# Kernel optimization log

Measured on AMD Instinct MI355X. Metric: run time of the kernel, lower is better.

## Reference

```python
import jax, jax.numpy as jnp
import numpy as np

B, D = 1024, 768


def setup_inputs() -> dict:
    key = jax.random.key(0)
    k1, k2 = jax.random.split(key)
    image_features = jax.random.normal(k1, (B, D), dtype=jnp.float32)
    # plant a few exact duplicate rows so the label-propagation path is nontrivial
    image_features = image_features.at[17].set(image_features[3])
    image_features = image_features.at[512].set(image_features[3])
    image_features = image_features.at[900].set(image_features[128])
    text_features = jax.random.normal(k2, (B, D), dtype=jnp.float32)
    logit_scale = jnp.float32(14.285714)  # exp(log(1/0.07)), standard CLIP init
    return {"image_features": image_features, "text_features": text_features, "logit_scale": logit_scale}


def reference(image_features, text_features, logit_scale):
    # logits_per_image: [B, B]
    logits = logit_scale * (image_features @ text_features.T)
    # Duplicate detection: the original O(B^2) python loop assigns to row j the
    # index of the FIRST row i (i <= j) whose features exactly equal row j.
    # eq[i, j] = rows i and j are elementwise identical
    eq = jnp.all(image_features[:, None, :] == image_features[None, :, :], axis=-1)  # [B, B] bool
    labels = jnp.argmax(eq, axis=0)  # first matching index per row (diag guarantees a hit)
    # cross-entropy with integer labels, mean over batch
    logp = jax.nn.log_softmax(logits, axis=1)
    loss = -jnp.mean(jnp.take_along_axis(logp, labels[:, None], axis=1))
    return loss
```

## Files before the change

kernel.cpp:

```cpp
#include <hip/hip_runtime.h>
#include <stdint.h>

#define BATCH 1024
#define DIM 768

typedef unsigned long long u64;
typedef __attribute__((ext_vector_type(8))) short short8;
typedef __attribute__((ext_vector_type(4))) float f32x4;

#define WS_TAIL     0
#define WS_PMAX  4096
#define WS_PSUM 20480
#define WS_LVAL 36864
#define WS_TXTB 49152

__device__ __forceinline__ unsigned short to_bf16(float x) {
    unsigned int u = __float_as_uint(x);
    return (unsigned short)((u + 0x7FFFu + ((u >> 16) & 1u)) >> 16);
}

__global__ __launch_bounds__(256) void prep_kernel(
        const float* __restrict__ txt, int* __restrict__ tailcnt,
        unsigned short* __restrict__ txtB) {
    if (blockIdx.x == 0 && threadIdx.x == 0) { *tailcnt = 0; }
    const int wave = threadIdx.x >> 6;
    const int lane = threadIdx.x & 63;

    for (int i = wave; i < 6; i += 4) {
        const int G  = blockIdx.x * 6 + i;
        const int tt = G / 24;
        const int g  = G - tt * 24;
        const int col = tt * 16 + (lane & 15);
        const int k0  = g * 32 + (lane >> 4) * 8;
        const float4 va = *(const float4*)(txt + (size_t)col * DIM + k0);
        const float4 vb = *(const float4*)(txt + (size_t)col * DIM + k0 + 4);
        short8 hv = {(short)to_bf16(va.x), (short)to_bf16(va.y),
                     (short)to_bf16(va.z), (short)to_bf16(va.w),
                     (short)to_bf16(vb.x), (short)to_bf16(vb.y),
                     (short)to_bf16(vb.z), (short)to_bf16(vb.w)};
        *(short8*)(txtB + (size_t)(g * 64 + tt) * 512 + lane * 8) = hv;
    }
}

__global__ __launch_bounds__(1024) void gemm_fused(
        const float* __restrict__ img, const float* __restrict__ txt,
        const float* __restrict__ scale_p, const unsigned short* __restrict__ txtB,
        float* __restrict__ pmax, float* __restrict__ psum,
        float* __restrict__ lval, int* __restrict__ tailcnt,
        float* __restrict__ out) {
    __shared__ unsigned short Ahi[16 * DIM];
    __shared__ float logitsS[16 * 260];
    __shared__ int isLast;
    __shared__ float part[16];

    const int tid  = threadIdx.x;
    const int wave = tid >> 6;
    const int lane = tid & 63;
    const int quad = lane >> 4;
    const int l15  = lane & 15;
    const int r0    = (blockIdx.x >> 2) * 16;
    const int chunk = blockIdx.x & 3;

    {
        const float* ir = img + (size_t)(r0 + wave) * DIM;
#pragma unroll
        for (int j = 0; j < 12; ++j) {
            const int k = lane + j * 64;
            Ahi[((k >> 3) * 16 + wave) * 8 + (k & 7)] = to_bf16(ir[k]);
        }
    }
    __syncthreads();

    const int t = chunk * 16 + wave;
    const int foff = quad * 128 + l15 * 8;
    f32x4 acc = {0.f, 0.f, 0.f, 0.f};
#pragma unroll
    for (int kk = 0; kk < 24; ++kk) {
        const short8 a = *(const short8*)&Ahi[kk * 512 + foff];
        const short8 b = *(const short8*)(txtB + (size_t)(kk * 64 + t) * 512 + foff);
        acc = __builtin_amdgcn_mfma_f32_16x16x32_bf16(a, b, acc, 0, 0, 0);
    }

    const float scale = scale_p[0];
#pragma unroll
    for (int r = 0; r < 4; ++r)
        logitsS[(quad * 4 + r) * 260 + wave * 16 + l15] = scale * acc[r];
    __syncthreads();

    {
        const float4 f = *(const float4*)&logitsS[wave * 260 + lane * 4];
        float mx = fmaxf(fmaxf(f.x, f.y), fmaxf(f.z, f.w));
#pragma unroll
        for (int s = 32; s; s >>= 1) mx = fmaxf(mx, __shfl_xor(mx, s, 64));
        float sum = __expf(f.x - mx) + __expf(f.y - mx) +
                    __expf(f.z - mx) + __expf(f.w - mx);
#pragma unroll
        for (int s = 32; s; s >>= 1) sum += __shfl_xor(sum, s, 64);
        if (lane == 0) {
            atomicExch(&pmax[(r0 + wave) * 4 + chunk], mx);
            atomicExch(&psum[(r0 + wave) * 4 + chunk], sum);
        }
    }

    if (wave < 4) {
        const int j = r0 + chunk * 4 + wave;
        const float2 sj = *(const float2*)(img + (size_t)j * DIM);
        int lo = -1;
        int label = j;
        for (;;) {
            int cand = BATCH;
#pragma unroll
            for (int it = 0; it < 16; ++it) {
                const int i = lane + it * 64;
                const float2 si = *(const float2*)(img + (size_t)i * DIM);
                if (i < j && i > lo && si.x == sj.x && si.y == sj.y)
                    cand = min(cand, i);
            }
#pragma unroll
            for (int s = 32; s; s >>= 1) cand = min(cand, __shfl_xor(cand, s, 64));
            if (cand >= j) break;
            const float4* rpm = (const float4*)(img + (size_t)cand * DIM);
            const float4* rpj = (const float4*)(img + (size_t)j * DIM);
            bool eq = true;
#pragma unroll
            for (int cc = 0; cc < 3; ++cc) {
                float4 vm = rpm[cc * 64 + lane];
                float4 vj = rpj[cc * 64 + lane];
                eq = eq && (vm.x == vj.x) && (vm.y == vj.y) &&
                     (vm.z == vj.z) && (vm.w == vj.w);
            }
            if (__all(eq)) { label = cand; break; }
            lo = cand;
        }

        const float4* aj = (const float4*)(img + (size_t)j * DIM);
        const float4* bl = (const float4*)(txt + (size_t)label * DIM);
        float s = 0.0f;
#pragma unroll
        for (int cc = 0; cc < 3; ++cc) {
            const float4 va = aj[cc * 64 + lane];
            const float4 vb = bl[cc * 64 + lane];
            s += va.x * vb.x + va.y * vb.y + va.z * vb.z + va.w * vb.w;
        }
#pragma unroll
        for (int m = 32; m; m >>= 1) s += __shfl_xor(s, m, 64);
        if (lane == 0) atomicExch(&lval[j], scale * s);
    }

    __syncthreads();
    if (tid == 0)
        isLast = (atomicAdd(tailcnt, 1) == (int)gridDim.x - 1) ? 1 : 0;
    __syncthreads();
    if (!isLast) return;
    __threadfence();

    {
        const float4 m4 = *(const float4*)&pmax[tid * 4];
        const float4 s4 = *(const float4*)&psum[tid * 4];
        const float lv = lval[tid];
        const float gmax = fmaxf(fmaxf(m4.x, m4.y), fmaxf(m4.z, m4.w));
        const float ss = s4.x * __expf(m4.x - gmax) + s4.y * __expf(m4.y - gmax)
                       + s4.z * __expf(m4.z - gmax) + s4.w * __expf(m4.w - gmax);
        float loss = gmax + __logf(ss) - lv;
#pragma unroll
        for (int m = 32; m; m >>= 1) loss += __shfl_xor(loss, m, 64);
        if (lane == 0) part[wave] = loss;
        __syncthreads();
        if (tid == 0) {
            float tot = 0.0f;
#pragma unroll
            for (int w = 0; w < 16; ++w) tot += part[w];
            out[0] = tot * (1.0f / BATCH);
        }
    }
}

extern "C" void kernel_launch(void* const* d_in, const int* in_sizes, int n_in,
                              void* d_out, int out_size, void* d_ws, size_t ws_size,
                              hipStream_t stream) {
    const float* img   = (const float*)d_in[0];
    const float* txt   = (const float*)d_in[1];
    const float* scale = (const float*)d_in[2];
    float* out = (float*)d_out;
    char* ws = (char*)d_ws;

    int*   tailcnt = (int*)(ws + WS_TAIL);
    float* pmax    = (float*)(ws + WS_PMAX);
    float* psum    = (float*)(ws + WS_PSUM);
    float* lval    = (float*)(ws + WS_LVAL);
    unsigned short* txtB = (unsigned short*)(ws + WS_TXTB);

    prep_kernel<<<256, 256, 0, stream>>>(txt, tailcnt, txtB);
    gemm_fused<<<256, 1024, 0, stream>>>(img, txt, scale, txtB,
                                         pmax, psum, lval, tailcnt, out);
}
```

Measured before the change: 78.07 us.

## Move label search to prep kernel and finalize loss per row via atomics

The duplicate-row label search and the label-logit dot product move from the GEMM kernel into the prep kernel, so the GEMM blocks only do the MFMA and the partial softmax. The single last-block tail reduction is replaced by per-row atomic counters. The fourth chunk to finish a row combines the partials, adds that row's loss into a global accumulator, and the final row writes the mean. This removes the serialized tail block and shortens the critical path of the GEMM kernel, but it adds many global atomics and makes the sum order nondeterministic.

```diff
diff --git a/kernel.cpp b/kernel.cpp
--- a/kernel.cpp
+++ b/kernel.cpp
@@ -8,23 +8,40 @@
 typedef __attribute__((ext_vector_type(8))) short short8;
 typedef __attribute__((ext_vector_type(4))) float f32x4;
 
-#define WS_TAIL     0
-#define WS_PMAX  4096
-#define WS_PSUM 20480
-#define WS_LVAL 36864
-#define WS_TXTB 49152
+#define WS_ACC      0
+#define WS_RDC      8
+#define WS_ROWCNT 4096
+#define WS_PMAX  12288
+#define WS_PSUM  28672
+#define WS_LVAL  45056
+#define WS_TXTB  49152
 
 __device__ __forceinline__ unsigned short to_bf16(float x) {
     unsigned int u = __float_as_uint(x);
     return (unsigned short)((u + 0x7FFFu + ((u >> 16) & 1u)) >> 16);
 }
 
+__device__ __forceinline__ float atomic_read_f32(float* p) {
+    unsigned int v = atomicOr((unsigned int*)p, 0u);
+    return __uint_as_float(v);
+}
+
 __global__ __launch_bounds__(256) void prep_kernel(
-        const float* __restrict__ txt, int* __restrict__ tailcnt,
-        unsigned short* __restrict__ txtB) {
-    if (blockIdx.x == 0 && threadIdx.x == 0) { *tailcnt = 0; }
+        const float* __restrict__ img, const float* __restrict__ txt,
+        const float* __restrict__ scale_p,
+        unsigned short* __restrict__ txtB, float* __restrict__ lval,
+        float* __restrict__ acc, int* __restrict__ rowdonecnt,
+        int* __restrict__ rowcnt) {
     const int wave = threadIdx.x >> 6;
     const int lane = threadIdx.x & 63;
+
+    if (blockIdx.x == 0) {
+        rowcnt[threadIdx.x * 4 + 0] = 0;
+        rowcnt[threadIdx.x * 4 + 1] = 0;
+        rowcnt[threadIdx.x * 4 + 2] = 0;
+        rowcnt[threadIdx.x * 4 + 3] = 0;
+        if (threadIdx.x == 0) { *acc = 0.0f; *rowdonecnt = 0; }
+    }
 
     for (int i = wave; i < 6; i += 4) {
         const int G  = blockIdx.x * 6 + i;
@@ -40,18 +57,62 @@
                      (short)to_bf16(vb.z), (short)to_bf16(vb.w)};
         *(short8*)(txtB + (size_t)(g * 64 + tt) * 512 + lane * 8) = hv;
     }
+
+    {
+        const int j = blockIdx.x * 4 + wave;
+        const float2 sj = *(const float2*)(img + (size_t)j * DIM);
+        int lo = -1;
+        int label = j;
+        for (;;) {
+            int cand = BATCH;
+#pragma unroll
+            for (int it = 0; it < 16; ++it) {
+                const int i = lane + it * 64;
+                const float2 si = *(const float2*)(img + (size_t)i * DIM);
+                if (i < j && i > lo && si.x == sj.x && si.y == sj.y)
+                    cand = min(cand, i);
+            }
+#pragma unroll
+            for (int s = 32; s; s >>= 1) cand = min(cand, __shfl_xor(cand, s, 64));
+            if (cand >= j) break;
+            const float4* rpm = (const float4*)(img + (size_t)cand * DIM);
+            const float4* rpj = (const float4*)(img + (size_t)j * DIM);
+            bool eq = true;
+#pragma unroll
+            for (int cc = 0; cc < 3; ++cc) {
+                float4 vm = rpm[cc * 64 + lane];
+                float4 vj = rpj[cc * 64 + lane];
+                eq = eq && (vm.x == vj.x) && (vm.y == vj.y) &&
+                     (vm.z == vj.z) && (vm.w == vj.w);
+            }
+            if (__all(eq)) { label = cand; break; }
+            lo = cand;
+        }
+
+        const float4* aj = (const float4*)(img + (size_t)j * DIM);
+        const float4* bl = (const float4*)(txt + (size_t)label * DIM);
+        float s = 0.0f;
+#pragma unroll
+        for (int cc = 0; cc < 3; ++cc) {
+            const float4 va = aj[cc * 64 + lane];
+            const float4 vb = bl[cc * 64 + lane];
+            s += va.x * vb.x + va.y * vb.y + va.z * vb.z + va.w * vb.w;
+        }
+#pragma unroll
+        for (int m = 32; m; m >>= 1) s += __shfl_xor(s, m, 64);
+        if (lane == 0) atomicExch(&lval[j], scale_p[0] * s);
+    }
 }
 
 __global__ __launch_bounds__(1024) void gemm_fused(
-        const float* __restrict__ img, const float* __restrict__ txt,
-        const float* __restrict__ scale_p, const unsigned short* __restrict__ txtB,
+        const float* __restrict__ img, const float* __restrict__ scale_p,
+        const unsigned short* __restrict__ txtB,
         float* __restrict__ pmax, float* __restrict__ psum,
-        float* __restrict__ lval, int* __restrict__ tailcnt,
+        float* __restrict__ lval, float* __restrict__ acc,
+        int* __restrict__ rowdonecnt, int* __restrict__ rowcnt,
         float* __restrict__ out) {
     __shared__ unsigned short Ahi[16 * DIM];
     __shared__ float logitsS[16 * 260];
-    __shared__ int isLast;
-    __shared__ float part[16];
 
     const int tid  = threadIdx.x;
     const int wave = tid >> 6;
@@ -73,104 +134,56 @@
 
     const int t = chunk * 16 + wave;
     const int foff = quad * 128 + l15 * 8;
-    f32x4 acc = {0.f, 0.f, 0.f, 0.f};
+    f32x4 a4 = {0.f, 0.f, 0.f, 0.f};
 #pragma unroll
     for (int kk = 0; kk < 24; ++kk) {
         const short8 a = *(const short8*)&Ahi[kk * 512 + foff];
         const short8 b = *(const short8*)(txtB + (size_t)(kk * 64 + t) * 512 + foff);
-        acc = __builtin_amdgcn_mfma_f32_16x16x32_bf16(a, b, acc, 0, 0, 0);
+        a4 = __builtin_amdgcn_mfma_f32_16x16x32_bf16(a, b, a4, 0, 0, 0);
     }
 
     const float scale = scale_p[0];
 #pragma unroll
     for (int r = 0; r < 4; ++r)
-        logitsS[(quad * 4 + r) * 260 + wave * 16 + l15] = scale * acc[r];
+        logitsS[(quad * 4 + r) * 260 + wave * 16 + l15] = scale * a4[r];
     __syncthreads();
 
-    {
-        const float4 f = *(const float4*)&logitsS[wave * 260 + lane * 4];
-        float mx = fmaxf(fmaxf(f.x, f.y), fmaxf(f.z, f.w));
-#pragma unroll
-        for (int s = 32; s; s >>= 1) mx = fmaxf(mx, __shfl_xor(mx, s, 64));
-        float sum = __expf(f.x - mx) + __expf(f.y - mx) +
-                    __expf(f.z - mx) + __expf(f.w - mx);
-#pragma unroll
-        for (int s = 32; s; s >>= 1) sum += __shfl_xor(sum, s, 64);
-        if (lane == 0) {
-            atomicExch(&pmax[(r0 + wave) * 4 + chunk], mx);
-            atomicExch(&psum[(r0 + wave) * 4 + chunk], sum);
-        }
-    }
-
-    if (wave < 4) {
-        const int j = r0 + chunk * 4 + wave;
-        const float2 sj = *(const float2*)(img + (size_t)j * DIM);
-        int lo = -1;
-        int label = j;
-        for (;;) {
-            int cand = BATCH;
-#pragma unroll
-            for (int it = 0; it < 16; ++it) {
-                const int i = lane + it * 64;
-                const float2 si = *(const float2*)(img + (size_t)i * DIM);
-                if (i < j && i > lo && si.x == sj.x && si.y == sj.y)
-                    cand = min(cand, i);
-            }
-#pragma unroll
-            for (int s = 32; s; s >>= 1) cand = min(cand, __shfl_xor(cand, s, 64));
-            if (cand >= j) break;
-            const float4* rpm = (const float4*)(img + (size_t)cand * DIM);
-            const float4* rpj = (const float4*)(img + (size_t)j * DIM);
-            bool eq = true;
-#pragma unroll
-            for (int cc = 0; cc < 3; ++cc) {
-                float4 vm = rpm[cc * 64 + lane];
-                float4 vj = rpj[cc * 64 + lane];
-                eq = eq && (vm.x == vj.x) && (vm.y == vj.y) &&
-                     (vm.z == vj.z) && (vm.w == vj.w);
-            }
-            if (__all(eq)) { label = cand; break; }
-            lo = cand;
-        }
-
-        const float4* aj = (const float4*)(img + (size_t)j * DIM);
-        const float4* bl = (const float4*)(txt + (size_t)label * DIM);
-        float s = 0.0f;
-#pragma unroll
-        for (int cc = 0; cc < 3; ++cc) {
-            const float4 va = aj[cc * 64 + lane];
-            const float4 vb = bl[cc * 64 + lane];
-            s += va.x * vb.x + va.y * vb.y + va.z * vb.z + va.w * vb.w;
-        }
-#pragma unroll
-        for (int m = 32; m; m >>= 1) s += __shfl_xor(s, m, 64);
-        if (lane == 0) atomicExch(&lval[j], scale * s);
-    }
-
-    __syncthreads();
-    if (tid == 0)
-        isLast = (atomicAdd(tailcnt, 1) == (int)gridDim.x - 1) ? 1 : 0;
-    __syncthreads();
-    if (!isLast) return;
-    __threadfence();
-
-    {
-        const float4 m4 = *(const float4*)&pmax[tid * 4];
-        const float4 s4 = *(const float4*)&psum[tid * 4];
-        const float lv = lval[tid];
-        const float gmax = fmaxf(fmaxf(m4.x, m4.y), fmaxf(m4.z, m4.w));
-        const float ss = s4.x * __expf(m4.x - gmax) + s4.y * __expf(m4.y - gmax)
-                       + s4.z * __expf(m4.z - gmax) + s4.w * __expf(m4.w - gmax);
-        float loss = gmax + __logf(ss) - lv;
-#pragma unroll
-        for (int m = 32; m; m >>= 1) loss += __shfl_xor(loss, m, 64);
-        if (lane == 0) part[wave] = loss;
-        __syncthreads();
-        if (tid == 0) {
-            float tot = 0.0f;
-#pragma unroll
-            for (int w = 0; w < 16; ++w) tot += part[w];
-            out[0] = tot * (1.0f / BATCH);
+    const float4 f = *(const float4*)&logitsS[wave * 260 + lane * 4];
+    float mx = fmaxf(fmaxf(f.x, f.y), fmaxf(f.z, f.w));
+#pragma unroll
+    for (int s = 32; s; s >>= 1) mx = fmaxf(mx, __shfl_xor(mx, s, 64));
+    float sum = __expf(f.x - mx) + __expf(f.y - mx) +
+                __expf(f.z - mx) + __expf(f.w - mx);
+#pragma unroll
+    for (int s = 32; s; s >>= 1) sum += __shfl_xor(sum, s, 64);
+
+    if (lane == 0) {
+        const int row = r0 + wave;
+        const float o1 = atomicExch(&pmax[row * 4 + chunk], mx);
+        const float o2 = atomicExch(&psum[row * 4 + chunk], sum);
+        asm volatile("" :: "v"(o1), "v"(o2));
+        const int old = atomicAdd(&rowcnt[row], 1);
+        if (old == 3) {
+            float pm[4], ps[4];
+#pragma unroll
+            for (int c = 0; c < 4; ++c) {
+                pm[c] = atomic_read_f32(&pmax[row * 4 + c]);
+                ps[c] = atomic_read_f32(&psum[row * 4 + c]);
+            }
+            const float lv = lval[row];
+            const float gmax = fmaxf(fmaxf(pm[0], pm[1]), fmaxf(pm[2], pm[3]));
+            const float ss = ps[0] * __expf(pm[0] - gmax)
+                           + ps[1] * __expf(pm[1] - gmax)
+                           + ps[2] * __expf(pm[2] - gmax)
+                           + ps[3] * __expf(pm[3] - gmax);
+            const float loss = gmax + __logf(ss) - lv;
+            const float ao = atomicAdd(acc, loss);
+            asm volatile("" :: "v"(ao));
+            const int dold = atomicAdd(rowdonecnt, 1);
+            if (dold == (int)BATCH - 1) {
+                const float tot = atomicAdd(acc, 0.0f);
+                out[0] = tot * (1.0f / BATCH);
+            }
         }
     }
 }
@@ -184,13 +197,17 @@
     float* out = (float*)d_out;
     char* ws = (char*)d_ws;
 
-    int*   tailcnt = (int*)(ws + WS_TAIL);
-    float* pmax    = (float*)(ws + WS_PMAX);
-    float* psum    = (float*)(ws + WS_PSUM);
-    float* lval    = (float*)(ws + WS_LVAL);
+    float* acc        = (float*)(ws + WS_ACC);
+    int*   rowdonecnt = (int*)(ws + WS_RDC);
+    int*   rowcnt     = (int*)(ws + WS_ROWCNT);
+    float* pmax       = (float*)(ws + WS_PMAX);
+    float* psum       = (float*)(ws + WS_PSUM);
+    float* lval       = (float*)(ws + WS_LVAL);
     unsigned short* txtB = (unsigned short*)(ws + WS_TXTB);
 
-    prep_kernel<<<256, 256, 0, stream>>>(txt, tailcnt, txtB);
-    gemm_fused<<<256, 1024, 0, stream>>>(img, txt, scale, txtB,
-                                         pmax, psum, lval, tailcnt, out);
-}
+    prep_kernel<<<256, 256, 0, stream>>>(img, txt, scale, txtB, lval,
+                                         acc, rowdonecnt, rowcnt);
+    gemm_fused<<<256, 1024, 0, stream>>>(img, scale, txtB,
+                                         pmax, psum, lval, acc,
+                                         rowdonecnt, rowcnt, out);
+}
```

Result: slower. 101.2 us (+29.7%).

## Compute full logit rows per block and reduce loss via global atomic accumulator

Applied to the files above, without the earlier changes.

The grid shrinks from 256 to 64 blocks, and each block now computes all 1024 columns for its 16 rows, with each wave holding four MFMA accumulators. The row log-sum-exp and label loss are finished inside the block. The pmax/psum/lval round trip through global memory and the last-block tail pass are gone; block partial losses are summed with a float atomicAdd and a done counter. The cost is that only 64 of the GPU's compute units are used, and the float atomic sum runs in nondeterministic order.

```diff
diff --git a/kernel.cpp b/kernel.cpp
--- a/kernel.cpp
+++ b/kernel.cpp
@@ -3,15 +3,14 @@
 
 #define BATCH 1024
 #define DIM 768
+#define NBLK 64
 
 typedef unsigned long long u64;
 typedef __attribute__((ext_vector_type(8))) short short8;
 typedef __attribute__((ext_vector_type(4))) float f32x4;
 
-#define WS_TAIL     0
-#define WS_PMAX  4096
-#define WS_PSUM 20480
-#define WS_LVAL 36864
+#define WS_ACC      0
+#define WS_DONE     8
 #define WS_TXTB 49152
 
 __device__ __forceinline__ unsigned short to_bf16(float x) {
@@ -20,9 +19,9 @@
 }
 
 __global__ __launch_bounds__(256) void prep_kernel(
-        const float* __restrict__ txt, int* __restrict__ tailcnt,
-        unsigned short* __restrict__ txtB) {
-    if (blockIdx.x == 0 && threadIdx.x == 0) { *tailcnt = 0; }
+        const float* __restrict__ txt, float* __restrict__ acc,
+        int* __restrict__ donecnt, unsigned short* __restrict__ txtB) {
+    if (blockIdx.x == 0 && threadIdx.x == 0) { *acc = 0.0f; *donecnt = 0; }
     const int wave = threadIdx.x >> 6;
     const int lane = threadIdx.x & 63;
 
@@ -42,15 +41,15 @@
     }
 }
 
+#define LSTRIDE 1036
+
 __global__ __launch_bounds__(1024) void gemm_fused(
         const float* __restrict__ img, const float* __restrict__ txt,
         const float* __restrict__ scale_p, const unsigned short* __restrict__ txtB,
-        float* __restrict__ pmax, float* __restrict__ psum,
-        float* __restrict__ lval, int* __restrict__ tailcnt,
+        float* __restrict__ acc_g, int* __restrict__ donecnt,
         float* __restrict__ out) {
     __shared__ unsigned short Ahi[16 * DIM];
-    __shared__ float logitsS[16 * 260];
-    __shared__ int isLast;
+    __shared__ float logitsS[16][LSTRIDE];
     __shared__ float part[16];
 
     const int tid  = threadIdx.x;
@@ -58,8 +57,7 @@
     const int lane = tid & 63;
     const int quad = lane >> 4;
     const int l15  = lane & 15;
-    const int r0    = (blockIdx.x >> 2) * 16;
-    const int chunk = blockIdx.x & 3;
+    const int r0   = blockIdx.x * 16;
 
     {
         const float* ir = img + (size_t)(r0 + wave) * DIM;
@@ -71,24 +69,32 @@
     }
     __syncthreads();
 
-    const int t = chunk * 16 + wave;
     const int foff = quad * 128 + l15 * 8;
-    f32x4 acc = {0.f, 0.f, 0.f, 0.f};
+    f32x4 acc[4] = {{0.f,0.f,0.f,0.f},{0.f,0.f,0.f,0.f},
+                    {0.f,0.f,0.f,0.f},{0.f,0.f,0.f,0.f}};
 #pragma unroll
     for (int kk = 0; kk < 24; ++kk) {
         const short8 a = *(const short8*)&Ahi[kk * 512 + foff];
-        const short8 b = *(const short8*)(txtB + (size_t)(kk * 64 + t) * 512 + foff);
-        acc = __builtin_amdgcn_mfma_f32_16x16x32_bf16(a, b, acc, 0, 0, 0);
+#pragma unroll
+        for (int q = 0; q < 4; ++q) {
+            const int tt = wave * 4 + q;
+            const short8 b = *(const short8*)(txtB + (size_t)(kk * 64 + tt) * 512 + foff);
+            acc[q] = __builtin_amdgcn_mfma_f32_16x16x32_bf16(a, b, acc[q], 0, 0, 0);
+        }
     }
 
     const float scale = scale_p[0];
 #pragma unroll
-    for (int r = 0; r < 4; ++r)
-        logitsS[(quad * 4 + r) * 260 + wave * 16 + l15] = scale * acc[r];
+    for (int q = 0; q < 4; ++q)
+#pragma unroll
+        for (int r = 0; r < 4; ++r)
+            logitsS[quad * 4 + r][wave * 64 + q * 16 + l15] = scale * acc[q][r];
     __syncthreads();
 
-    {
-        const float4 f = *(const float4*)&logitsS[wave * 260 + lane * 4];
+    float pm[4], ps[4];
+#pragma unroll
+    for (int c = 0; c < 4; ++c) {
+        const float4 f = *(const float4*)&logitsS[wave][c * 256 + lane * 4];
         float mx = fmaxf(fmaxf(f.x, f.y), fmaxf(f.z, f.w));
 #pragma unroll
         for (int s = 32; s; s >>= 1) mx = fmaxf(mx, __shfl_xor(mx, s, 64));
@@ -96,14 +102,16 @@
                     __expf(f.z - mx) + __expf(f.w - mx);
 #pragma unroll
         for (int s = 32; s; s >>= 1) sum += __shfl_xor(sum, s, 64);
-        if (lane == 0) {
-            atomicExch(&pmax[(r0 + wave) * 4 + chunk], mx);
-            atomicExch(&psum[(r0 + wave) * 4 + chunk], sum);
-        }
+        pm[c] = mx; ps[c] = sum;
     }
+    const float gmax = fmaxf(fmaxf(pm[0], pm[1]), fmaxf(pm[2], pm[3]));
+    const float ss = ps[0] * __expf(pm[0] - gmax) + ps[1] * __expf(pm[1] - gmax)
+                   + ps[2] * __expf(pm[2] - gmax) + ps[3] * __expf(pm[3] - gmax);
+    const float lse = gmax + __logf(ss);
 
-    if (wave < 4) {
-        const int j = r0 + chunk * 4 + wave;
+    const int j = r0 + wave;
+    float loss;
+    {
         const float2 sj = *(const float2*)(img + (size_t)j * DIM);
         int lo = -1;
         int label = j;
@@ -144,32 +152,20 @@
         }
 #pragma unroll
         for (int m = 32; m; m >>= 1) s += __shfl_xor(s, m, 64);
-        if (lane == 0) atomicExch(&lval[j], scale * s);
+        loss = lse - scale * s;
     }
 
+    if (lane == 0) part[wave] = loss;
     __syncthreads();
-    if (tid == 0)
-        isLast = (atomicAdd(tailcnt, 1) == (int)gridDim.x - 1) ? 1 : 0;
-    __syncthreads();
-    if (!isLast) return;
-    __threadfence();
-
-    {
-        const float4 m4 = *(const float4*)&pmax[tid * 4];
-        const float4 s4 = *(const float4*)&psum[tid * 4];
-        const float lv = lval[tid];
-        const float gmax = fmaxf(fmaxf(m4.x, m4.y), fmaxf(m4.z, m4.w));
-        const float ss = s4.x * __expf(m4.x - gmax) + s4.y * __expf(m4.y - gmax)
-                       + s4.z * __expf(m4.z - gmax) + s4.w * __expf(m4.w - gmax);
-        float loss = gmax + __logf(ss) - lv;
+    if (tid == 0) {
+        float bl = 0.0f;
 #pragma unroll
-        for (int m = 32; m; m >>= 1) loss += __shfl_xor(loss, m, 64);
-        if (lane == 0) part[wave] = loss;
-        __syncthreads();
-        if (tid == 0) {
-            float tot = 0.0f;
-#pragma unroll
-            for (int w = 0; w < 16; ++w) tot += part[w];
+        for (int w = 0; w < 16; ++w) bl += part[w];
+        const float ao = atomicAdd(acc_g, bl);
+        asm volatile("" :: "v"(ao));
+        const int old = atomicAdd(donecnt, 1);
+        if (old == NBLK - 1) {
+            const float tot = atomicAdd(acc_g, 0.0f);
             out[0] = tot * (1.0f / BATCH);
         }
     }
@@ -184,13 +180,11 @@
     float* out = (float*)d_out;
     char* ws = (char*)d_ws;
 
-    int*   tailcnt = (int*)(ws + WS_TAIL);
-    float* pmax    = (float*)(ws + WS_PMAX);
-    float* psum    = (float*)(ws + WS_PSUM);
-    float* lval    = (float*)(ws + WS_LVAL);
+    float* acc     = (float*)(ws + WS_ACC);
+    int*   donecnt = (int*)(ws + WS_DONE);
     unsigned short* txtB = (unsigned short*)(ws + WS_TXTB);
 
-    prep_kernel<<<256, 256, 0, stream>>>(txt, tailcnt, txtB);
-    gemm_fused<<<256, 1024, 0, stream>>>(img, txt, scale, txtB,
-                                         pmax, psum, lval, tailcnt, out);
+    prep_kernel<<<256, 256, 0, stream>>>(txt, acc, donecnt, txtB);
+    gemm_fused<<<NBLK, 1024, 0, stream>>>(img, txt, scale, txtB,
+                                          acc, donecnt, out);
 }
```

After: 106.4 us. +36.3%, slower.
